# Kernel tuning notes

Hardware: AMD Instinct MI355X
Metric: run time of the kernel (lower is better)

Reference implementation:

```python
import jax, jax.numpy as jnp
import numpy as np

N_NODES = 65536
VOCAB = 1000
IN_DIM = 256
MEM_DIM = 256
HIDDEN = 256
NUM_CLASSES = 2


def _rand_parents(rng, n):
    # parent[i] < i for i >= 1 ; node 0 is the root (parent entry unused/masked)
    p = np.zeros(n, dtype=np.int64)
    p[1:] = rng.integers(0, np.arange(1, n))
    return jnp.asarray(p, dtype=jnp.int32)


def setup_inputs() -> dict:
    key = jax.random.key(0)
    ks = jax.random.split(key, 16)
    rng = np.random.default_rng(0)
    s = 0.05
    return {
        "l_tokens": jax.random.randint(ks[0], (N_NODES,), 0, VOCAB, dtype=jnp.int32),
        "l_parent": _rand_parents(rng, N_NODES),
        "r_tokens": jax.random.randint(ks[1], (N_NODES,), 0, VOCAB, dtype=jnp.int32),
        "r_parent": _rand_parents(rng, N_NODES),
        "emb_W": jax.random.normal(ks[2], (VOCAB, IN_DIM), jnp.float32) * s,
        "Wioux": jax.random.normal(ks[3], (IN_DIM, 3 * MEM_DIM), jnp.float32) * s,
        "bioux": jax.random.normal(ks[4], (3 * MEM_DIM,), jnp.float32) * s,
        "Wiouh": jax.random.normal(ks[5], (MEM_DIM, 3 * MEM_DIM), jnp.float32) * s,
        "biouh": jax.random.normal(ks[6], (3 * MEM_DIM,), jnp.float32) * s,
        "Wfx": jax.random.normal(ks[7], (IN_DIM, MEM_DIM), jnp.float32) * s,
        "bfx": jax.random.normal(ks[8], (MEM_DIM,), jnp.float32) * s,
        "Wfh": jax.random.normal(ks[9], (MEM_DIM, MEM_DIM), jnp.float32) * s,
        "bfh": jax.random.normal(ks[10], (MEM_DIM,), jnp.float32) * s,
        "Wh": jax.random.normal(ks[11], (2 * MEM_DIM, HIDDEN), jnp.float32) * s,
        "bh": jax.random.normal(ks[12], (HIDDEN,), jnp.float32) * s,
        "Wp": jax.random.normal(ks[13], (HIDDEN, NUM_CLASSES), jnp.float32) * s,
        "bp": jax.random.normal(ks[14], (NUM_CLASSES,), jnp.float32) * s,
    }


def _tree_lstm_root_c(tokens, parent, emb_W, Wioux, bioux, Wiouh, biouh,
                      Wfx, bfx, Wfh, bfh):
    # Batched x-dependent projections (faithful: ioux(emb), fx(emb))
    X = emb_W[tokens]                       # [N, in_dim]
    ioux_all = X @ Wioux + bioux            # [N, 3M]
    fx_all = X @ Wfx + bfx                  # [N, M]
    n = tokens.shape[0]
    m = Wfh.shape[0]

    def step(carry, i):
        h_sum, fc_sum, c_root = carry
        # ChildSumTreeLSTM.node_forward for node i
        iou = ioux_all[i] + h_sum[i] @ Wiouh + biouh
        ig, og, ug = jnp.split(iou, 3)
        c = jax.nn.sigmoid(ig) * jnp.tanh(ug) + fc_sum[i]   # leaf: fc_sum=0, h_sum=0
        h = jax.nn.sigmoid(og) * jnp.tanh(c)
        # forget-gate contribution of node i to its parent p:
        p = parent[i]
        f = jax.nn.sigmoid(h @ Wfh + bfh + fx_all[p])
        mask = (i != 0).astype(h.dtype)      # root has no parent
        h_sum = h_sum.at[p].add(h * mask)
        fc_sum = fc_sum.at[p].add(f * c * mask)
        c_root = jnp.where(i == 0, c, c_root)
        return (h_sum, fc_sum, c_root), None

    init = (jnp.zeros((n, m), X.dtype), jnp.zeros((n, m), X.dtype),
            jnp.zeros((m,), X.dtype))
    # children-before-parents order: descending index (parent[i] < i)
    (h_sum, fc_sum, c_root), _ = jax.lax.scan(step, init, jnp.arange(n - 1, -1, -1))
    return c_root                            # lstate == root cell state c


def reference(l_tokens, l_parent, r_tokens, r_parent, emb_W, Wioux, bioux,
              Wiouh, biouh, Wfx, bfx, Wfh, bfh, Wh, bh, Wp, bp):
    cl = _tree_lstm_root_c(l_tokens, l_parent, emb_W, Wioux, bioux, Wiouh,
                           biouh, Wfx, bfx, Wfh, bfh)
    cr = _tree_lstm_root_c(r_tokens, r_parent, emb_W, Wioux, bioux, Wiouh,
                           biouh, Wfx, bfx, Wfh, bfh)
    # Similarity head on root cell states
    vec = jnp.concatenate([cl * cr, jnp.abs(cl - cr)])[None, :]  # [1, 2M]
    hid = jax.nn.sigmoid(vec @ Wh + bh)
    return jax.nn.softmax(hid @ Wp + bp, axis=1)                 # [1, num_classes]
```

## Files before the change

kernel.cpp:

```cpp
#include <hip/hip_runtime.h>
#include <math.h>

#define NN 65536
#define TWO_N (2 * NN)
#define VOCAB 1000
#define MD 256
#define G3 768
#define DMAX 65536
#define HALF (DMAX / 2)
#define DCAP 128
#define NB 64
#define NT 256
#define NTS 1024
#define NSPAN 1024
#define SPAN 128
#define NTEAMS 64

typedef __attribute__((ext_vector_type(8))) short bf16x8;
typedef __attribute__((ext_vector_type(4))) float f32x4;

struct Params {
    const int* l_tokens; const int* l_parent;
    const int* r_tokens; const int* r_parent;
    const float* emb_W;
    const float* Wioux; const float* bioux;
    const float* Wiouh; const float* biouh;
    const float* Wfx;   const float* bfx;
    const float* Wfh;   const float* bfh;
    const float* Wh;    const float* bh;
    const float* Wp;    const float* bp;
    float* out;
    float* E_ioux;
    float* E_fx;
    float* C_leaf;
    float* H_leaf;
    float* FH_leaf;
    unsigned int* Wiouh_p;
    unsigned int* Wfh_p;
    float* h_sum;
    float* fc_sum;
    float* c_root;
    unsigned short* hstage;
    int* tarr;
    unsigned long long* ad_a;
    unsigned long long* ad_b;
    int* hc;
    int* pending;
    int* pend2;
    int* rank;
    int* lstart;
    int* blocksum;
    int* cnt; int* offs; int* cur;
    int* order;
    int* lorder;
    int* gtab;
    int* gdb;
    int* ecut;
    int* dbase;
    int* maxd;
    int cap_rows;
};

struct SWT {
    unsigned int wiou[12 * 2048];
    unsigned short hbufA[NB * MD];
    int nid[2][NB]; int row[2][NB]; int prow[2][NB];
    int tok[2][NB]; int ptok[2][NB]; int pgid[2][NB];
};

__device__ __forceinline__ float sigmoidf_(float x) {
    return 1.0f / (1.0f + __expf(-x));
}
__device__ __forceinline__ float tanhf_(float x) {
    float ex = __expf(2.0f * x);
    return 1.0f - 2.0f / (ex + 1.0f);
}
__device__ __forceinline__ unsigned int bf16rne_(float x) {
    unsigned int b = __float_as_uint(x);
    return (b + 0x7FFFu + ((b >> 16) & 1u)) >> 16;
}
__device__ __forceinline__ int aload_(int* p) {
    return __hip_atomic_load(p, __ATOMIC_RELAXED, __HIP_MEMORY_SCOPE_AGENT);
}
__device__ __forceinline__ float acohf_(const float* p) {
    return __hip_atomic_load((float*)p, __ATOMIC_RELAXED,
                             __HIP_MEMORY_SCOPE_AGENT);
}
__device__ __forceinline__ unsigned long long acohu64_(const void* p) {
    return __hip_atomic_load((unsigned long long*)p, __ATOMIC_RELAXED,
                             __HIP_MEMORY_SCOPE_AGENT);
}
__device__ __forceinline__ int dep_(const Params& P, int g) {
    return ((const int*)P.ad_a)[2 * g];
}
__device__ __forceinline__ int rowr(const Params& P, int tree, int d, int lr) {
    int r = P.dbase[tree * HALF + d] + lr;
    if (r >= P.cap_rows) r -= P.cap_rows;
    return r;
}

__global__ __launch_bounds__(NT) void k_prep(Params P) {
    __shared__ float es[4][MD];
    const int t = threadIdx.x, bid = blockIdx.x, nblk = gridDim.x;
    const int gsize = nblk * NT, gtid = bid * NT + t;
    for (int u = gtid; u < 48 * 2048; u += gsize) {
        int tl = u >> 11, rem = u & 2047;
        int kb = rem >> 8, rem2 = rem & 255;
        int ln = rem2 >> 2, jj = (rem2 & 3) << 1;
        int k = kb * 32 + (ln >> 4) * 8 + jj;
        int n = tl * 16 + (ln & 15);
        float x0 = P.Wiouh[(size_t)k * G3 + n];
        float x1 = P.Wiouh[(size_t)(k + 1) * G3 + n];
        P.Wiouh_p[u] = bf16rne_(x0) | (bf16rne_(x1) << 16);
    }
    for (int u = gtid; u < 16 * 2048; u += gsize) {
        int tl = u >> 11, rem = u & 2047;
        int kb = rem >> 8, rem2 = rem & 255;
        int ln = rem2 >> 2, jj = (rem2 & 3) << 1;
        int k = kb * 32 + (ln >> 4) * 8 + jj;
        int n = tl * 16 + (ln & 15);
        float x0 = P.Wfh[(size_t)k * MD + n];
        float x1 = P.Wfh[(size_t)(k + 1) * MD + n];
        P.Wfh_p[u] = bf16rne_(x0) | (bf16rne_(x1) << 16);
    }
    for (int v0 = bid * 4; v0 < VOCAB; v0 += nblk * 4) {
        __syncthreads();
        #pragma unroll
        for (int r = 0; r < 4; ++r)
            es[r][t] = (v0 + r < VOCAB) ? P.emb_W[(size_t)(v0 + r) * MD + t] : 0.f;
        __syncthreads();
        float a0[4] = {0.f,0.f,0.f,0.f}, a1[4] = {0.f,0.f,0.f,0.f};
        float a2[4] = {0.f,0.f,0.f,0.f}, a3[4] = {0.f,0.f,0.f,0.f};
        for (int k = 0; k < MD; ++k) {
            float wi = P.Wioux[k * G3 + t];
            float wo = P.Wioux[k * G3 + 256 + t];
            float wu = P.Wioux[k * G3 + 512 + t];
            float wf = P.Wfx[k * MD + t];
            #pragma unroll
            for (int r = 0; r < 4; ++r) {
                float e = es[r][k];
                a0[r] += wi * e; a1[r] += wo * e; a2[r] += wu * e; a3[r] += wf * e;
            }
        }
        float bi = P.bioux[t], bo = P.bioux[256 + t], bu = P.bioux[512 + t], bf = P.bfx[t];
        float hb_i = P.biouh[t], hb_o = P.biouh[256 + t], hb_u = P.biouh[512 + t];
        __syncthreads();
        for (int r = 0; r < 4; ++r) {
            float hl = 0.f;
            if (v0 + r < VOCAB) {
                float ei = a0[r] + bi, eo = a1[r] + bo, eu = a2[r] + bu;
                P.E_ioux[(size_t)(v0 + r) * G3 + t]       = ei;
                P.E_ioux[(size_t)(v0 + r) * G3 + 256 + t] = eo;
                P.E_ioux[(size_t)(v0 + r) * G3 + 512 + t] = eu;
                P.E_fx[(size_t)(v0 + r) * MD + t]         = a3[r] + bf;
                float cl = sigmoidf_(ei + hb_i) * tanhf_(eu + hb_u);
                hl = sigmoidf_(eo + hb_o) * tanhf_(cl);
                P.C_leaf[(size_t)(v0 + r) * MD + t] = cl;
                P.H_leaf[(size_t)(v0 + r) * MD + t] = hl;
            }
            es[r][t] = hl;
        }
        __syncthreads();
        float af[4] = {0.f,0.f,0.f,0.f};
        for (int k = 0; k < MD; ++k) {
            float wf = P.Wfh[(size_t)k * MD + t];
            #pragma unroll
            for (int r = 0; r < 4; ++r) af[r] += wf * es[r][k];
        }
        for (int r = 0; r < 4; ++r)
            if (v0 + r < VOCAB) P.FH_leaf[(size_t)(v0 + r) * MD + t] = af[r];
        __syncthreads();
    }
    for (int g = gtid; g < TWO_N; g += gsize) {
        int tree = g >> 16, i = g & (NN - 1);
        if (i == 0) {
            P.ad_a[g] = ((unsigned long long)g << 32);
        } else {
            const int* par = tree ? P.r_parent : P.l_parent;
            int pg = (tree << 16) | par[i];
            P.ad_a[g] = ((unsigned long long)pg << 32) | 1ull;
            P.hc[pg] = 1;
        }
    }
}

__global__ __launch_bounds__(NT) void k_double(Params P, int it) {
    const int gtid = blockIdx.x * NT + threadIdx.x;
    const int gsize = gridDim.x * NT;
    if (it == 0) {
        for (int g = gtid; g < TWO_N; g += gsize) {
            int i = g & (NN - 1);
            if (i != 0 && !P.hc[g]) {
                int tree = g >> 16;
                const int* par = tree ? P.r_parent : P.l_parent;
                atomicAdd(&P.pending[(tree << 16) | par[i]], 1);
            }
        }
    }
    unsigned long long* pa = (it & 1) ? P.ad_b : P.ad_a;
    unsigned long long* q  = (it & 1) ? P.ad_a : P.ad_b;
    for (int g = gtid; g < TWO_N; g += gsize) {
        if (!P.hc[g]) continue;
        unsigned long long v = pa[g];
        unsigned long long va = pa[v >> 32];
        q[g] = (va & 0xFFFFFFFF00000000ull)
             | (unsigned long long)((unsigned int)v + (unsigned int)va);
    }
}

__global__ __launch_bounds__(NT) void k_s1(Params P) {
    __shared__ int hcnt[2 * DCAP];
    __shared__ int hmax2[2];
    const int t = threadIdx.x, bid = blockIdx.x, nblk = gridDim.x;
    const int gsize = nblk * NT, gtid = bid * NT + t;
    for (int i = t; i < 2 * DCAP; i += NT) hcnt[i] = 0;
    if (t < 2) hmax2[t] = 0;
    __syncthreads();
    for (int g = gtid; g < TWO_N; g += gsize) {
        if (!P.hc[g]) continue;
        int tree = g >> 16;
        int d = dep_(P, g);
        if (d < DCAP) {
            atomicAdd(&hcnt[tree * DCAP + d], 1);
            atomicMax(&hmax2[tree], d);
        } else {
            atomicAdd(&P.cnt[tree * DMAX + d], 1);
            atomicMax(&P.maxd[tree], d);
        }
    }
    __syncthreads();
    for (int i = t; i < 2 * DCAP; i += NT) {
        int c = hcnt[i];
        if (c > 0) atomicAdd(&P.cnt[(i >= DCAP ? DMAX : 0) + (i & (DCAP - 1))], c);
    }
    if (t < 2) atomicMax(&P.maxd[t], hmax2[t]);
    for (int sp = bid; sp < NSPAN; sp += nblk) {
        __syncthreads();
        if (t < SPAN) hcnt[t] = P.pending[sp * SPAN + t];
        __syncthreads();
        for (int off = 1; off < SPAN; off <<= 1) {
            int a = (t >= off && t < SPAN) ? hcnt[t - off] : 0;
            __syncthreads();
            if (t < SPAN) hcnt[t] += a;
            __syncthreads();
        }
        if (t == SPAN - 1) P.blocksum[sp] = hcnt[t];
    }
}

__global__ __launch_bounds__(NT) void k_s2(Params P) {
    __shared__ int hcnt[NT];
    const int t = threadIdx.x;
    int4 v = ((const int4*)P.blocksum)[t];
    int s4 = v.x + v.y + v.z + v.w;
    hcnt[t] = s4;
    __syncthreads();
    for (int off = 1; off < NT; off <<= 1) {
        int a = (t >= off) ? hcnt[t - off] : 0;
        __syncthreads();
        hcnt[t] += a;
        __syncthreads();
    }
    int excl = t ? hcnt[t - 1] : 0;
    int4 r;
    r.x = excl; r.y = r.x + v.x; r.z = r.y + v.y; r.w = r.z + v.z;
    ((int4*)P.blocksum)[t] = r;
    if (t == NT - 1) P.maxd[23] = hcnt[NT - 1];
    __syncthreads();
    if (t < 2) {
        int tree = t;
        int run = tree * NN;
        int md = P.maxd[tree];
        for (int d = 0; d <= md; ++d) {
            P.offs[tree * DMAX + d] = run;
            run += P.cnt[tree * DMAX + d];
        }
    }
    __syncthreads();
    int md0 = P.maxd[0], md1 = P.maxd[1];
    int smax = md0 > md1 ? md0 : md1;
    if (t == 0) {
        long p = 0;
        for (int d = smax; d >= 0; --d) {
            P.dbase[d] = (int)(p % (long)P.cap_rows);
            p += P.cnt[d];
            P.dbase[HALF + d] = (int)(p % (long)P.cap_rows);
            p += P.cnt[DMAX + d];
        }
        int e = 0, hi = smax;
        while (hi >= 0) {
            long s = (long)(P.cnt[hi] + P.cnt[DMAX + hi]);
            if (hi > 0) s += P.cnt[hi - 1] + P.cnt[DMAX + hi - 1];
            int lo = hi;
            while (lo > 0) {
                long add = (lo - 1 > 0)
                    ? (P.cnt[lo - 2] + P.cnt[DMAX + lo - 2]) : 0;
                if (s + add > (long)P.cap_rows) break;
                s += add; --lo;
            }
            P.ecut[e++] = lo;
            hi = lo - 1;
        }
        P.maxd[24] = e;
        int j = 0;
        for (int d = smax; d >= 0; --d) {
            P.gdb[d] = j;
            j += (P.cnt[d] + NB - 1) / NB + (P.cnt[DMAX + d] + NB - 1) / NB;
        }
        P.maxd[22] = j;
    }
    __syncthreads();
    for (int d = t; d <= smax; d += NT) {
        int j = P.gdb[d];
        for (int tr = 0; tr < 2; ++tr) {
            int mdt = tr ? md1 : md0;
            int n = (d <= mdt) ? P.cnt[tr * DMAX + d] : 0;
            int st = P.offs[tr * DMAX + d];
            for (int b = 0; b < n; b += NB) {
                int cv = n - b; if (cv > NB) cv = NB;
                P.gtab[j++] = (st + b) | (cv << 20);
            }
        }
    }
}

__global__ __launch_bounds__(NT) void k_p2(Params P) {
    __shared__ int hcnt[NT];
    const int t = threadIdx.x, bid = blockIdx.x, nblk = gridDim.x;
    for (int sp = bid; sp < NSPAN; sp += nblk) {
        __syncthreads();
        if (t < SPAN) hcnt[t] = P.pending[sp * SPAN + t];
        __syncthreads();
        for (int off = 1; off < SPAN; off <<= 1) {
            int a = (t >= off && t < SPAN) ? hcnt[t - off] : 0;
            __syncthreads();
            if (t < SPAN) hcnt[t] += a;
            __syncthreads();
        }
        if (t < SPAN) {
            int excl = t ? hcnt[t - 1] : 0;
            P.lstart[sp * SPAN + t] = P.blocksum[sp] + excl;
        }
    }
}

__global__ __launch_bounds__(NT) void k_s3(Params P) {
    __shared__ int hcnt[2 * DCAP];
    __shared__ int hbase[2 * DCAP];
    const int t = threadIdx.x, bid = blockIdx.x, nblk = gridDim.x;
    const int gsize = nblk * NT, gtid = bid * NT + t;
    for (int i = t; i < 2 * DCAP; i += NT) hcnt[i] = 0;
    __syncthreads();
    for (int g = gtid; g < TWO_N; g += gsize) {
        if (!P.hc[g]) continue;
        int tree = g >> 16;
        int d = dep_(P, g);
        if (d < DCAP) atomicAdd(&hcnt[tree * DCAP + d], 1);
    }
    __syncthreads();
    for (int i = t; i < 2 * DCAP; i += NT) {
        int c = hcnt[i];
        if (c > 0) {
            int idx = (i >= DCAP ? DMAX : 0) + (i & (DCAP - 1));
            hbase[i] = P.offs[idx] + atomicAdd(&P.cur[idx], c);
        }
        hcnt[i] = 0;
    }
    __syncthreads();
    for (int g = gtid; g < TWO_N; g += gsize) {
        int tree = g >> 16, i = g & (NN - 1);
        if (P.hc[g]) {
            int d = dep_(P, g);
            if (d < DCAP) {
                int b = tree * DCAP + d;
                int pos = atomicAdd(&hcnt[b], 1);
                int gp = hbase[b] + pos;
                P.order[gp] = g;
                P.rank[g] = gp - P.offs[tree * DMAX + d];
            } else {
                int idx = tree * DMAX + d;
                int pos = atomicAdd(&P.cur[idx], 1);
                P.order[P.offs[idx] + pos] = g;
                P.rank[g] = pos;
            }
        } else if (i != 0) {
            const int* par = tree ? P.r_parent : P.l_parent;
            const int* toks = tree ? P.r_tokens : P.l_tokens;
            int pg = (tree << 16) | par[i];
            int pos = __hip_atomic_fetch_add(&P.pending[pg], -1,
                          __ATOMIC_RELAXED, __HIP_MEMORY_SCOPE_AGENT) - 1;
            P.lorder[P.lstart[pg] + pos] = toks[i];
        }
    }
}

__global__ __launch_bounds__(NT) void k_seed(Params P, int e) {
    const int t = threadIdx.x, bid = blockIdx.x, nblk = gridDim.x;
    int nep = P.maxd[24];
    if (e >= nep) return;
    int md0 = P.maxd[0], md1 = P.maxd[1];
    int smax = md0 > md1 ? md0 : md1;
    int hi = smax;
    for (int k = 0; k < e; ++k) hi = P.ecut[k] - 1;
    int lo = P.ecut[e];
    int sa = (lo > 0) ? lo - 1 : 0;
    int sb = (e == 0) ? hi : hi - 1;
    if (sa <= sb) {
        float b_f = P.bfh[t];
        for (int tree = 0; tree < 2; ++tree) {
            int mdt = tree ? md1 : md0;
            int bb = sb < mdt ? sb : mdt;
            if (sa > bb) continue;
            int st = P.offs[tree * DMAX + sa];
            int en = P.offs[tree * DMAX + bb] + P.cnt[tree * DMAX + bb];
            for (int idx = st + bid; idx < en; idx += nblk) {
                int g = P.order[idx];
                int i = g & (NN - 1);
                int tok = (tree ? P.r_tokens : P.l_tokens)[i];
                int d = dep_(P, g);
                int row = rowr(P, tree, d, P.rank[g]);
                int ls = P.lstart[g];
                int le = (g + 1 < TWO_N) ? P.lstart[g + 1] : P.maxd[23];
                float efx = P.E_fx[(size_t)tok * MD + t] + b_f;
                float ha = 0.f, fa = 0.f;
                for (int k = ls; k < le; ++k) {
                    int lt = P.lorder[k];
                    ha += P.H_leaf[(size_t)lt * MD + t];
                    fa += sigmoidf_(P.FH_leaf[(size_t)lt * MD + t] + efx)
                          * P.C_leaf[(size_t)lt * MD + t];
                }
                P.h_sum[(size_t)row * MD + t] = ha;
                P.fc_sum[(size_t)row * MD + t] = fa;
            }
        }
    }
    if (e == 0) {
        const int gsize = nblk * NT, gtid = bid * NT + t;
        for (int g = gtid; g < TWO_N; g += gsize) {
            int i = g & (NN - 1);
            if (i != 0 && P.hc[g]) {
                int tree = g >> 16;
                const int* par = tree ? P.r_parent : P.l_parent;
                int pg = (tree << 16) | par[i];
                atomicAdd(&P.pending[pg], 4);
                atomicAdd(&P.pend2[pg], 4);
            }
        }
    }
}

__device__ __forceinline__ void load_meta(const Params& P, SWT& sm, int jj,
                                          int buf, int t) {
    if (t < NB) {
        int g = -1, row = 0, prow = 0, tok = 0, ptok = 0, pgid = 0;
        int en = P.gtab[jj];
        int base = en & 0xFFFFF, cntv = en >> 20;
        if (t < cntv) {
            g = P.order[base + t];
            int tree = g >> 16, i = g & (NN - 1);
            const int* toks = tree ? P.r_tokens : P.l_tokens;
            const int* pars = tree ? P.r_parent : P.l_parent;
            tok = toks[i];
            int d = dep_(P, g);
            row = rowr(P, tree, d, P.rank[g]);
            if (i != 0) {
                int pl = pars[i];
                ptok = toks[pl];
                pgid = (tree << 16) | pl;
                prow = rowr(P, tree, d - 1, P.rank[pgid]);
            }
        }
        sm.nid[buf][t] = g; sm.row[buf][t] = row; sm.prow[buf][t] = prow;
        sm.tok[buf][t] = tok; sm.ptok[buf][t] = ptok; sm.pgid[buf][t] = pgid;
    }
}

__global__ __launch_bounds__(NTS, 1) void k_sweep(Params P, int e) {
    __shared__ SWT sm;
    int nep = P.maxd[24];
    if (e >= nep) return;
    const int t = threadIdx.x;
    const int b4 = blockIdx.x & 3;
    const int team = blockIdx.x >> 2;
    const int nteams = gridDim.x >> 2;
    const int wv = t >> 6;
    const int l = t & 63, lr = l >> 4, nloc = l & 15;

    for (int u = t; u < 12 * 2048; u += NTS) {
        int lt = u >> 11;
        int gate = lt >> 2, wq = lt & 3;
        sm.wiou[u] = P.Wiouh_p[(size_t)(gate * 16 + b4 * 4 + wq) * 2048 + (u & 2047)];
    }

    int md0 = P.maxd[0], md1 = P.maxd[1];
    int smax = md0 > md1 ? md0 : md1;
    int hi = smax;
    for (int k = 0; k < e; ++k) hi = P.ecut[k] - 1;
    int lo = P.ecut[e];
    int GT = P.maxd[22];
    int jend = (lo > 0) ? P.gdb[lo - 1] : GT;

    const unsigned short* Wl = (const unsigned short*)sm.wiou;
    const unsigned short* Wfg = (const unsigned short*)P.Wfh_p;
    int* tarr = P.tarr + e * NTEAMS + team;
    int kloc = 0;
    int cur = 0;

    const int j0 = P.gdb[hi] + team;
    if (j0 < jend) load_meta(P, sm, j0, 0, t);

    for (int j = j0; j < jend; j += nteams, ++kloc) {
        int en = P.gtab[j];
        int cntv = en >> 20;
        int nrb = (cntv + 15) >> 4;
        int ntask = nrb * 4;
        if (t < NB) {
            int g = sm.nid[cur][t];
            if (g >= 0) {
                while (aload_(&P.pending[g]) != 0) __builtin_amdgcn_s_sleep(4);
            }
        }
        __syncthreads();

        const int mtot2 = (nrb << 4) * (MD / 2);
        for (int u = t; u < mtot2; u += NTS) {
            int m = u >> 7, c2 = (u & 127) << 1;
            unsigned int pk = 0;
            if (sm.nid[cur][m] >= 0) {
                unsigned long long d2 =
                    acohu64_(&P.h_sum[(size_t)sm.row[cur][m] * MD + c2]);
                float v0 = __uint_as_float((unsigned int)d2);
                float v1 = __uint_as_float((unsigned int)(d2 >> 32));
                pk = bf16rne_(v0) | (bf16rne_(v1) << 16);
            }
            *(unsigned int*)&sm.hbufA[m * MD + (c2 ^ ((m & 7) << 3))] = pk;
        }
        __syncthreads();

        f32x4 aiv, aov, auv;
        float crg[4];
        const int tt = wv;
        const int rb = tt >> 2, q = tt & 3;
        const int n = (b4 * 4 + q) * 16 + nloc;
        if (tt < ntask) {
            float b_i = P.biouh[n], b_o = P.biouh[256 + n], b_u = P.biouh[512 + n];
            #pragma unroll
            for (int r = 0; r < 4; ++r) {
                int m = rb * 16 + lr * 4 + r;
                float vi = 0.f, vo = 0.f, vu = 0.f;
                if (sm.nid[cur][m] >= 0) {
                    const float* Ei = P.E_ioux + (size_t)sm.tok[cur][m] * G3 + n;
                    vi = Ei[0] + b_i;
                    vo = Ei[256] + b_o;
                    vu = Ei[512] + b_u;
                }
                aiv[r] = vi; aov[r] = vo; auv[r] = vu;
            }
            #pragma unroll
            for (int kb = 0; kb < 8; ++kb) {
                int idx = (rb * 16 + nloc) * MD +
                          ((kb * 32 + lr * 8) ^ ((nloc & 7) << 3));
                bf16x8 afr = *(const bf16x8*)&sm.hbufA[idx];
                bf16x8 bi = *(const bf16x8*)&Wl[((q) * 8 + kb) * 512 + l * 8];
                bf16x8 bo = *(const bf16x8*)&Wl[((4 + q) * 8 + kb) * 512 + l * 8];
                bf16x8 bu = *(const bf16x8*)&Wl[((8 + q) * 8 + kb) * 512 + l * 8];
                aiv = __builtin_amdgcn_mfma_f32_16x16x32_bf16(afr, bi, aiv, 0, 0, 0);
                aov = __builtin_amdgcn_mfma_f32_16x16x32_bf16(afr, bo, aov, 0, 0, 0);
                auv = __builtin_amdgcn_mfma_f32_16x16x32_bf16(afr, bu, auv, 0, 0, 0);
            }
        }

        if (t < NB) {
            int g = sm.nid[cur][t];
            if (g >= 0) {
                while (aload_(&P.pend2[g]) != 0) __builtin_amdgcn_s_sleep(4);
            }
        }
        __syncthreads();

        unsigned short* hs = P.hstage
            + ((size_t)(team * 2 + (kloc & 1))) * (NB * MD);
        if (tt < ntask) {
            #pragma unroll
            for (int r = 0; r < 4; ++r) {
                int m = rb * 16 + lr * 4 + r;
                int g = sm.nid[cur][m];
                float c = 0.f, h = 0.f;
                if (g >= 0) {
                    float fcv = acohf_(&P.fc_sum[(size_t)sm.row[cur][m] * MD + n]);
                    c = sigmoidf_(aiv[r]) * tanhf_(auv[r]) + fcv;
                    h = sigmoidf_(aov[r]) * tanhf_(c);
                    int i = g & (NN - 1);
                    if (i == 0) {
                        P.c_root[(g >> 16) * MD + n] = c;
                    } else {
                        atomicAdd(&P.h_sum[(size_t)sm.prow[cur][m] * MD + n], h);
                    }
                }
                __hip_atomic_store(&hs[m * MD + n],
                                   (unsigned short)bf16rne_(h),
                                   __ATOMIC_RELAXED, __HIP_MEMORY_SCOPE_AGENT);
                crg[r] = c;
            }
        }

        __syncthreads();
        if (t < NB) {
            if (t == 0) {
                __hip_atomic_fetch_add(tarr, 1, __ATOMIC_RELAXED,
                                       __HIP_MEMORY_SCOPE_AGENT);
            }
            int g = sm.nid[cur][t];
            if (g >= 0 && (g & (NN - 1)) != 0) {
                __hip_atomic_fetch_add(&P.pending[sm.pgid[cur][t]], -1,
                                       __ATOMIC_RELAXED, __HIP_MEMORY_SCOPE_AGENT);
            }
        }
        if (j + nteams < jend) load_meta(P, sm, j + nteams, cur ^ 1, t);
        if (t == 0) {
            while (aload_(tarr) < 4 * (kloc + 1)) __builtin_amdgcn_s_sleep(2);
        }
        __syncthreads();

        const unsigned long long* hs64 = (const unsigned long long*)hs;
        if (tt < ntask) {
            float b_f = P.bfh[n];
            f32x4 af;
            #pragma unroll
            for (int r = 0; r < 4; ++r) {
                int m = rb * 16 + lr * 4 + r;
                int g = sm.nid[cur][m];
                float v = 0.f;
                if (g >= 0 && (g & (NN - 1)) != 0)
                    v = b_f + P.E_fx[(size_t)sm.ptok[cur][m] * MD + n];
                af[r] = v;
            }
            #pragma unroll
            for (int kb = 0; kb < 8; ++kb) {
                union { unsigned long long u[2]; bf16x8 v; } hu;
                int u0 = ((rb * 16 + nloc) * 128 + (kb * 32 + lr * 8) / 2) >> 1;
                hu.u[0] = acohu64_(&hs64[u0]);
                hu.u[1] = acohu64_(&hs64[u0 + 1]);
                bf16x8 bf = *(const bf16x8*)&Wfg[(((b4 * 4 + q) * 8 + kb) * 64 + l) * 8];
                af = __builtin_amdgcn_mfma_f32_16x16x32_bf16(hu.v, bf, af, 0, 0, 0);
            }
            #pragma unroll
            for (int r = 0; r < 4; ++r) {
                int m = rb * 16 + lr * 4 + r;
                int g = sm.nid[cur][m];
                if (g >= 0 && (g & (NN - 1)) != 0) {
                    atomicAdd(&P.fc_sum[(size_t)sm.prow[cur][m] * MD + n],
                              sigmoidf_(af[r]) * crg[r]);
                }
            }
        }

        __syncthreads();
        if (t < NB) {
            int g = sm.nid[cur][t];
            if (g >= 0 && (g & (NN - 1)) != 0) {
                __hip_atomic_fetch_add(&P.pend2[sm.pgid[cur][t]], -1,
                                       __ATOMIC_RELAXED, __HIP_MEMORY_SCOPE_AGENT);
            }
        }
        cur ^= 1;
    }
}

__global__ __launch_bounds__(NT) void k_head(Params P) {
    __shared__ float vec[2 * MD];
    __shared__ float red[2][NT];
    const int t = threadIdx.x;
    float cl = P.c_root[t], cr = P.c_root[MD + t];
    vec[t] = cl * cr;
    vec[MD + t] = fabsf(cl - cr);
    __syncthreads();
    float acc = 0.f;
    for (int j = 0; j < 2 * MD; ++j) acc += vec[j] * P.Wh[(size_t)j * MD + t];
    float hid = sigmoidf_(acc + P.bh[t]);
    red[0][t] = hid * P.Wp[t * 2 + 0];
    red[1][t] = hid * P.Wp[t * 2 + 1];
    __syncthreads();
    for (int s = 128; s > 0; s >>= 1) {
        if (t < s) {
            red[0][t] += red[0][t + s];
            red[1][t] += red[1][t + s];
        }
        __syncthreads();
    }
    if (t == 0) {
        float l0 = red[0][0] + P.bp[0];
        float l1 = red[1][0] + P.bp[1];
        float mx = fmaxf(l0, l1);
        float e0 = __expf(l0 - mx), e1 = __expf(l1 - mx);
        float inv = 1.0f / (e0 + e1);
        P.out[0] = e0 * inv;
        P.out[1] = e1 * inv;
    }
}

extern "C" void kernel_launch(void* const* d_in, const int* in_sizes, int n_in,
                              void* d_out, int out_size, void* d_ws, size_t ws_size,
                              hipStream_t stream) {
    Params P;
    P.l_tokens = (const int*)d_in[0];
    P.l_parent = (const int*)d_in[1];
    P.r_tokens = (const int*)d_in[2];
    P.r_parent = (const int*)d_in[3];
    P.emb_W = (const float*)d_in[4];
    P.Wioux = (const float*)d_in[5];
    P.bioux = (const float*)d_in[6];
    P.Wiouh = (const float*)d_in[7];
    P.biouh = (const float*)d_in[8];
    P.Wfx   = (const float*)d_in[9];
    P.bfx   = (const float*)d_in[10];
    P.Wfh   = (const float*)d_in[11];
    P.bfh   = (const float*)d_in[12];
    P.Wh    = (const float*)d_in[13];
    P.bh    = (const float*)d_in[14];
    P.Wp    = (const float*)d_in[15];
    P.bp    = (const float*)d_in[16];
    P.out   = (float*)d_out;

    char* w = (char*)d_ws;
    auto alloc = [&](size_t bytes) {
        char* r = w;
        w += (bytes + 255) & ~(size_t)255;
        return r;
    };
    P.E_ioux   = (float*)alloc((size_t)VOCAB * G3 * 4);
    P.E_fx     = (float*)alloc((size_t)VOCAB * MD * 4);
    P.C_leaf   = (float*)alloc((size_t)VOCAB * MD * 4);
    P.H_leaf   = (float*)alloc((size_t)VOCAB * MD * 4);
    P.FH_leaf  = (float*)alloc((size_t)VOCAB * MD * 4);
    P.Wiouh_p  = (unsigned int*)alloc((size_t)48 * 2048 * 4);
    P.Wfh_p    = (unsigned int*)alloc((size_t)16 * 2048 * 4);
    P.c_root   = (float*)alloc(2 * MD * 4);
    P.hstage   = (unsigned short*)alloc((size_t)NTEAMS * 2 * NB * MD * 2);
    P.tarr     = (int*)alloc((size_t)8 * NTEAMS * 4);
    P.ad_a     = (unsigned long long*)alloc((size_t)TWO_N * 8);
    P.ad_b     = (unsigned long long*)alloc((size_t)TWO_N * 8);
    P.hc       = (int*)alloc((size_t)TWO_N * 4);
    P.pending  = (int*)alloc((size_t)TWO_N * 4);
    P.pend2    = (int*)alloc((size_t)TWO_N * 4);
    P.cnt      = (int*)alloc((size_t)2 * DMAX * 4);
    P.offs     = (int*)alloc((size_t)2 * DMAX * 4);
    P.cur      = (int*)alloc((size_t)2 * DMAX * 4);
    P.order    = (int*)alloc((size_t)TWO_N * 4);
    P.rank     = (int*)alloc((size_t)TWO_N * 4);
    P.lstart   = (int*)alloc((size_t)TWO_N * 4);
    P.lorder   = (int*)alloc((size_t)TWO_N * 4);
    P.blocksum = (int*)alloc((size_t)NSPAN * 4);
    P.gtab     = (int*)alloc((size_t)(TWO_N / 16 + 2 * DMAX + 256) * 4);
    P.gdb      = (int*)alloc((size_t)DMAX * 4);
    P.ecut     = (int*)alloc((size_t)DMAX * 4);
    P.dbase    = (int*)alloc((size_t)DMAX * 4);
    P.maxd     = (int*)alloc(256);

    size_t used = (size_t)(w - (char*)d_ws);
    size_t remain = (ws_size > used) ? (ws_size - used) : 0;
    size_t cap = remain / ((size_t)2 * MD * 4);
    if (cap > (size_t)TWO_N) cap = TWO_N;
    P.cap_rows = (int)cap;
    P.h_sum  = (float*)w;
    P.fc_sum = P.h_sum + cap * MD;

    hipMemsetAsync(P.hc, 0, (size_t)3 * TWO_N * 4, stream);
    hipMemsetAsync(P.cnt, 0, (size_t)3 * 2 * DMAX * 4, stream);
    hipMemsetAsync(P.maxd, 0, 256, stream);
    hipMemsetAsync(P.tarr, 0, (size_t)8 * NTEAMS * 4, stream);

    k_prep<<<dim3(512), dim3(NT), 0, stream>>>(P);
    for (int it = 0; it < 8; ++it)
        k_double<<<dim3(512), dim3(NT), 0, stream>>>(P, it);
    k_s1<<<dim3(NSPAN), dim3(NT), 0, stream>>>(P);
    k_s2<<<dim3(1), dim3(NT), 0, stream>>>(P);
    k_p2<<<dim3(NSPAN), dim3(NT), 0, stream>>>(P);
    k_s3<<<dim3(NSPAN), dim3(NT), 0, stream>>>(P);

    for (int e = 0; e < 6; ++e) {
        k_seed<<<dim3(1024), dim3(NT), 0, stream>>>(P, e);
        k_sweep<<<dim3(4 * NTEAMS), dim3(NTS), 0, stream>>>(P, e);
    }
    k_head<<<dim3(1), dim3(NT), 0, stream>>>(P);
}
```

Before: 912.3 us.

## Drop LDS weight staging, double sweep teams, fold prefix scan into s1

The sweep kernel no longer copies the W_iouh weight tile into shared memory and instead reads the packed weights straight from global memory, which shrinks LDS use. The launch bound now allows up to 8 blocks and the team count doubles to 128, aiming for more resident blocks working on the level-synchronous tree sweep. The per-span local prefix is written in k_s1, so k_p2 becomes a simple add of the block offsets instead of redoing the scan. The pointer-doubling pass count drops from 8 to 6, which risks incomplete depth computation for deep random trees. Global weight reads may also cost more latency than the LDS reads they replace.

Measured after the change: 1.211 ms. +32.7%, slower.

```diff
diff --git a/kernel.cpp b/kernel.cpp
--- a/kernel.cpp
+++ b/kernel.cpp
@@ -14,7 +14,7 @@
 #define NTS 1024
 #define NSPAN 1024
 #define SPAN 128
-#define NTEAMS 64
+#define NTEAMS 128
 
 typedef __attribute__((ext_vector_type(8))) short bf16x8;
 typedef __attribute__((ext_vector_type(4))) float f32x4;
@@ -62,7 +62,6 @@
 };
 
 struct SWT {
-    unsigned int wiou[12 * 2048];
     unsigned short hbufA[NB * MD];
     int nid[2][NB]; int row[2][NB]; int prow[2][NB];
     int tok[2][NB]; int ptok[2][NB]; int pgid[2][NB];
@@ -244,6 +243,10 @@
             if (t < SPAN) hcnt[t] += a;
             __syncthreads();
         }
+        if (t < SPAN) {
+            int excl = t ? hcnt[t - 1] : 0;
+            P.lstart[sp * SPAN + t] = excl;
+        }
         if (t == SPAN - 1) P.blocksum[sp] = hcnt[t];
     }
 }
@@ -325,23 +328,10 @@
 }
 
 __global__ __launch_bounds__(NT) void k_p2(Params P) {
-    __shared__ int hcnt[NT];
-    const int t = threadIdx.x, bid = blockIdx.x, nblk = gridDim.x;
-    for (int sp = bid; sp < NSPAN; sp += nblk) {
-        __syncthreads();
-        if (t < SPAN) hcnt[t] = P.pending[sp * SPAN + t];
-        __syncthreads();
-        for (int off = 1; off < SPAN; off <<= 1) {
-            int a = (t >= off && t < SPAN) ? hcnt[t - off] : 0;
-            __syncthreads();
-            if (t < SPAN) hcnt[t] += a;
-            __syncthreads();
-        }
-        if (t < SPAN) {
-            int excl = t ? hcnt[t - 1] : 0;
-            P.lstart[sp * SPAN + t] = P.blocksum[sp] + excl;
-        }
-    }
+    const int gtid = blockIdx.x * NT + threadIdx.x;
+    const int gsize = gridDim.x * NT;
+    for (int i = gtid; i < TWO_N; i += gsize)
+        P.lstart[i] += P.blocksum[i >> 7];
 }
 
 __global__ __launch_bounds__(NT) void k_s3(Params P) {
@@ -475,7 +465,7 @@
     }
 }
 
-__global__ __launch_bounds__(NTS, 1) void k_sweep(Params P, int e) {
+__global__ __launch_bounds__(NTS, 8) void k_sweep(Params P, int e) {
     __shared__ SWT sm;
     int nep = P.maxd[24];
     if (e >= nep) return;
@@ -486,12 +476,6 @@
     const int wv = t >> 6;
     const int l = t & 63, lr = l >> 4, nloc = l & 15;
 
-    for (int u = t; u < 12 * 2048; u += NTS) {
-        int lt = u >> 11;
-        int gate = lt >> 2, wq = lt & 3;
-        sm.wiou[u] = P.Wiouh_p[(size_t)(gate * 16 + b4 * 4 + wq) * 2048 + (u & 2047)];
-    }
-
     int md0 = P.maxd[0], md1 = P.maxd[1];
     int smax = md0 > md1 ? md0 : md1;
     int hi = smax;
@@ -500,7 +484,7 @@
     int GT = P.maxd[22];
     int jend = (lo > 0) ? P.gdb[lo - 1] : GT;
 
-    const unsigned short* Wl = (const unsigned short*)sm.wiou;
+    const unsigned short* Wg = (const unsigned short*)P.Wiouh_p;
     const unsigned short* Wfg = (const unsigned short*)P.Wfh_p;
     int* tarr = P.tarr + e * NTEAMS + team;
     int kloc = 0;
@@ -542,6 +526,7 @@
         const int tt = wv;
         const int rb = tt >> 2, q = tt & 3;
         const int n = (b4 * 4 + q) * 16 + nloc;
+        const int tq = b4 * 4 + q;
         if (tt < ntask) {
             float b_i = P.biouh[n], b_o = P.biouh[256 + n], b_u = P.biouh[512 + n];
             #pragma unroll
@@ -561,9 +546,9 @@
                 int idx = (rb * 16 + nloc) * MD +
                           ((kb * 32 + lr * 8) ^ ((nloc & 7) << 3));
                 bf16x8 afr = *(const bf16x8*)&sm.hbufA[idx];
-                bf16x8 bi = *(const bf16x8*)&Wl[((q) * 8 + kb) * 512 + l * 8];
-                bf16x8 bo = *(const bf16x8*)&Wl[((4 + q) * 8 + kb) * 512 + l * 8];
-                bf16x8 bu = *(const bf16x8*)&Wl[((8 + q) * 8 + kb) * 512 + l * 8];
+                bf16x8 bi = *(const bf16x8*)&Wg[(((tq) * 8 + kb) * 64 + l) * 8];
+                bf16x8 bo = *(const bf16x8*)&Wg[(((16 + tq) * 8 + kb) * 64 + l) * 8];
+                bf16x8 bu = *(const bf16x8*)&Wg[(((32 + tq) * 8 + kb) * 64 + l) * 8];
                 aiv = __builtin_amdgcn_mfma_f32_16x16x32_bf16(afr, bi, aiv, 0, 0, 0);
                 aov = __builtin_amdgcn_mfma_f32_16x16x32_bf16(afr, bo, aov, 0, 0, 0);
                 auv = __builtin_amdgcn_mfma_f32_16x16x32_bf16(afr, bu, auv, 0, 0, 0);
@@ -641,7 +626,7 @@
                 int u0 = ((rb * 16 + nloc) * 128 + (kb * 32 + lr * 8) / 2) >> 1;
                 hu.u[0] = acohu64_(&hs64[u0]);
                 hu.u[1] = acohu64_(&hs64[u0 + 1]);
-                bf16x8 bf = *(const bf16x8*)&Wfg[(((b4 * 4 + q) * 8 + kb) * 64 + l) * 8];
+                bf16x8 bf = *(const bf16x8*)&Wfg[((tq * 8 + kb) * 64 + l) * 8];
                 af = __builtin_amdgcn_mfma_f32_16x16x32_bf16(hu.v, bf, af, 0, 0, 0);
             }
             #pragma unroll
@@ -771,11 +756,11 @@
     hipMemsetAsync(P.tarr, 0, (size_t)8 * NTEAMS * 4, stream);
 
     k_prep<<<dim3(512), dim3(NT), 0, stream>>>(P);
-    for (int it = 0; it < 8; ++it)
+    for (int it = 0; it < 6; ++it)
         k_double<<<dim3(512), dim3(NT), 0, stream>>>(P, it);
     k_s1<<<dim3(NSPAN), dim3(NT), 0, stream>>>(P);
     k_s2<<<dim3(1), dim3(NT), 0, stream>>>(P);
-    k_p2<<<dim3(NSPAN), dim3(NT), 0, stream>>>(P);
+    k_p2<<<dim3(512), dim3(NT), 0, stream>>>(P);
     k_s3<<<dim3(NSPAN), dim3(NT), 0, stream>>>(P);
 
     for (int e = 0; e < 6; ++e) {
```
